# Kernel tuning notes

Measured on AMD Instinct MI355X. Metric: run time of the kernel, lower is better.

Reference implementation:

```python
import jax, jax.numpy as jnp
import numpy as np
from jax import lax

D_MODEL = 768
D_INNER = 1536   # expand * d_model
D_STATE = 16
D_CONV = 4
DT_RANK = 48     # ceil(768/16)
BATCH, SEQLEN = 2, 1024


def silu(x):
    return x * jax.nn.sigmoid(x)


def causal_conv1d(x, w, b):
    # x: (B, L, d)  w: (d, K) depthwise  b: (d,)
    # matches torch Conv1d(groups=d, padding=K-1)[..., :L]
    K = w.shape[1]
    L = x.shape[1]
    xp = jnp.pad(x, ((0, 0), (K - 1, 0), (0, 0)))
    out = b
    for k in range(K):
        out = out + xp[:, k:k + L, :] * w[:, k]
    return out


def mamba_branch(xz, conv_w, conv_b, x_proj_w, dt_proj_w, dt_bias, A_log, D):
    # xz: (B, L, 2*d_inner); faithful to mamba_inner_fn_no_out_proj
    x, z = jnp.split(xz, 2, axis=-1)
    x = silu(causal_conv1d(x, conv_w, conv_b))
    x_dbl = x @ x_proj_w.T                                  # (B,L,dt_rank+2N)
    dt, Bc, Cc = jnp.split(x_dbl, [DT_RANK, DT_RANK + D_STATE], axis=-1)
    delta = jax.nn.softplus(dt @ dt_proj_w.T + dt_bias)     # (B,L,d)
    A = -jnp.exp(A_log)                                     # (d,N)
    dA = jnp.exp(delta[..., None] * A)                      # (B,L,d,N)
    dBx = (delta * x)[..., None] * Bc[:, :, None, :]        # (B,L,d,N)

    def step(h, inp):
        da, dbx = inp
        h = da * h + dbx
        return h, h

    h0 = jnp.zeros((x.shape[0], x.shape[2], D_STATE), x.dtype)
    _, hs = lax.scan(step, h0, (jnp.swapaxes(dA, 0, 1), jnp.swapaxes(dBx, 0, 1)))
    y = jnp.einsum('lbdn,bln->bld', hs, Cc) + x * D         # (B,L,d)
    return y * silu(z)


def setup_inputs() -> dict:
    key = jax.random.key(0)
    ks = jax.random.split(key, 16)
    d, dm, n, r, K = D_INNER, D_MODEL, D_STATE, DT_RANK, D_CONV
    A_log = jnp.log(jnp.broadcast_to(jnp.arange(1, n + 1, dtype=jnp.float32), (d, n)))
    # faithful dt bias init: inverse-softplus of log-uniform dt in [1e-3, 1e-1]
    def dt_bias(k):
        dt = jnp.exp(jax.random.uniform(k, (d,)) * (np.log(0.1) - np.log(0.001)) + np.log(0.001))
        dt = jnp.clip(dt, 1e-4)
        return dt + jnp.log(-jnp.expm1(-dt))
    return {
        'hidden_states': jax.random.normal(ks[0], (BATCH, SEQLEN, dm), jnp.float32),
        'in_proj_w': jax.random.normal(ks[1], (2 * d, dm), jnp.float32) / np.sqrt(dm),
        'conv_w': jax.random.normal(ks[2], (d, K), jnp.float32) / np.sqrt(K),
        'conv_b': jax.random.normal(ks[3], (d,), jnp.float32) * 0.02,
        'x_proj_w': jax.random.normal(ks[4], (r + 2 * n, d), jnp.float32) / np.sqrt(d),
        'dt_proj_w': jax.random.uniform(ks[5], (d, r), jnp.float32, -r ** -0.5, r ** -0.5),
        'dt_proj_b': dt_bias(ks[6]),
        'A_log': A_log,
        'D': jnp.ones((d,), jnp.float32),
        'conv_w_b': jax.random.normal(ks[7], (d, K), jnp.float32) / np.sqrt(K),
        'conv_b_b': jax.random.normal(ks[8], (d,), jnp.float32) * 0.02,
        'x_proj_w_b': jax.random.normal(ks[9], (r + 2 * n, d), jnp.float32) / np.sqrt(d),
        'dt_proj_w_b': jax.random.uniform(ks[10], (d, r), jnp.float32, -r ** -0.5, r ** -0.5),
        'dt_proj_b_b': dt_bias(ks[11]),
        'A_b_log': A_log,
        'D_b': jnp.ones((d,), jnp.float32),
        'out_proj_w': jax.random.normal(ks[12], (dm, d), jnp.float32) / np.sqrt(d),
    }


def reference(hidden_states, in_proj_w, conv_w, conv_b, x_proj_w, dt_proj_w, dt_proj_b,
              A_log, D, conv_w_b, conv_b_b, x_proj_w_b, dt_proj_w_b, dt_proj_b_b,
              A_b_log, D_b, out_proj_w):
    # bimamba v2: forward scan + backward (flipped) scan, summed, then out_proj
    xz = hidden_states @ in_proj_w.T                        # (B,L,2*d_inner)
    out_f = mamba_branch(xz, conv_w, conv_b, x_proj_w, dt_proj_w, dt_proj_b, A_log, D)
    out_r = mamba_branch(xz[:, ::-1, :], conv_w_b, conv_b_b, x_proj_w_b,
                         dt_proj_w_b, dt_proj_b_b, A_b_log, D_b)[:, ::-1, :]
    return (out_f + out_r) @ out_proj_w.T                   # (B,L,d_model)
```

## Files before the change

kernel.cpp:

```cpp
#include <hip/hip_runtime.h>
#include <hip/hip_bf16.h>

#define LL 1024
#define DI 1536
#define N2 3072
#define ML 2048
#define CHUNKS 64
#define CLEN 16

typedef __attribute__((ext_vector_type(8))) short short8;
typedef __attribute__((ext_vector_type(4))) float f4;
typedef __attribute__((ext_vector_type(4))) float f32x4;

__device__ __forceinline__ ushort f2bf(float f) {
  union { float f; unsigned u; } v; v.f = f;
  unsigned u = v.u;
  u += 0x7fffu + ((u >> 16) & 1u);
  return (ushort)(u >> 16);
}
__device__ __forceinline__ float bf2f(ushort u) {
  union { unsigned i; float f; } w; w.i = ((unsigned)u) << 16; return w.f;
}
__device__ __forceinline__ f4 bf2f4(ushort4 u) {
  f4 r; r.x = bf2f(u.x); r.y = bf2f(u.y); r.z = bf2f(u.z); r.w = bf2f(u.w);
  return r;
}

__device__ __forceinline__ void gload16(const ushort* g, ushort* l) {
  __builtin_amdgcn_global_load_lds(
      (const __attribute__((address_space(1))) unsigned int*)g,
      (__attribute__((address_space(3))) unsigned int*)l, 16, 0, 0);
}

struct CvtSeg { const float* s; ushort* d; int n4; };
struct Cvt5 { CvtSeg seg[5]; };

#define CVT_BLOCKS 5232

__global__ void k_cvt(Cvt5 p, int total4,
                      const float* __restrict__ wf, const float* __restrict__ wb,
                      ushort* __restrict__ dtw) {
  int bid = blockIdx.x;
  if (bid < CVT_BLOCKS) {
    int i = bid * 256 + threadIdx.x;
    if (i >= total4) return;
    int off = i, sidx = 0;
    while (sidx < 4 && off >= p.seg[sidx].n4) { off -= p.seg[sidx].n4; ++sidx; }
    f4 v = *(const f4*)(p.seg[sidx].s + (size_t)off * 4);
    ushort4 o;
    o.x = f2bf(v.x); o.y = f2bf(v.y); o.z = f2bf(v.z); o.w = f2bf(v.w);
    *(ushort4*)(p.seg[sidx].d + (size_t)off * 4) = o;
  } else {
    int i = (bid - CVT_BLOCKS) * 256 + threadIdx.x;
    int c = i & 63;
    int rr = i >> 6;
    int dir = rr / 1536;
    int r = rr - dir * 1536;
    const float* w = dir ? wb : wf;
    dtw[i] = (c < 48) ? f2bf(w[r * 48 + c]) : (ushort)0;
  }
}

template<int EPI, bool NGUARD, int KS, bool OBF>
__global__ __launch_bounds__(256)
void k_gemm(const ushort* __restrict__ A, const ushort* __restrict__ Bm,
            void* __restrict__ Cp, int M, int N, int K,
            const float* __restrict__ bias, const float* __restrict__ bias2,
            size_t sA, size_t sB, size_t sC, size_t sKs, int kLen) {
  const int dir = blockIdx.z;
  A += (size_t)dir * sA;
  Bm += (size_t)dir * sB;
  size_t cbase = (size_t)dir * sC;
  const float* bp = (EPI == 1) ? (dir ? bias2 : bias) : nullptr;

  int n0, kOff, kEnd;
  if (KS > 1) {
    int yb_ = blockIdx.y;
    int nt = yb_ / KS, ks = yb_ - nt * KS;
    n0 = nt * 128;
    kOff = ks * kLen;
    kEnd = kOff + kLen;
    cbase += (size_t)ks * sKs;
  } else {
    n0 = blockIdx.y * 128;
    kOff = 0;
    kEnd = K;
  }

  __shared__ ushort As[128 * 32];
  __shared__ ushort Bs[128 * 32];
  const int tid = threadIdx.x;
  const int m0 = blockIdx.x * 128;
  const int wv = tid >> 6;
  const int lane = tid & 63;
  const int wr = (wv >> 1) * 64;
  const int wc = (wv & 1) * 64;
  const int lr = lane & 15;
  const int lk = lane >> 4;
  f32x4 acc[4][4] = {};
  for (int k0 = kOff; k0 < kEnd; k0 += 32) {
    #pragma unroll
    for (int i = 0; i < 2; ++i) {
      int e = (tid + i * 256) * 8;
      int r = e >> 5;
      int c = e & 31;
      gload16(A + (size_t)(m0 + r) * K + k0 + c, &As[(i * 256 + wv * 64) * 8]);
      gload16(Bm + (size_t)(n0 + r) * K + k0 + c, &Bs[(i * 256 + wv * 64) * 8]);
    }
    __syncthreads();
    short8 af[4], bfr[4];
    #pragma unroll
    for (int m = 0; m < 4; ++m) af[m] = *(const short8*)(&As[(wr + m*16 + lr) * 32 + lk*8]);
    #pragma unroll
    for (int n = 0; n < 4; ++n) bfr[n] = *(const short8*)(&Bs[(wc + n*16 + lr) * 32 + lk*8]);
    #pragma unroll
    for (int m = 0; m < 4; ++m)
      #pragma unroll
      for (int n = 0; n < 4; ++n)
        acc[m][n] = __builtin_amdgcn_mfma_f32_16x16x32_bf16(af[m], bfr[n], acc[m][n], 0, 0, 0);
    __syncthreads();
  }
  #pragma unroll
  for (int m = 0; m < 4; ++m) {
    int gr = m0 + wr + m * 16 + lk * 4;
    #pragma unroll
    for (int n = 0; n < 4; ++n) {
      int gc = n0 + wc + n * 16 + lr;
      if (NGUARD && gc >= N) continue;
      #pragma unroll
      for (int r = 0; r < 4; ++r) {
        float v = acc[m][n][r];
        if (EPI == 1) {
          v += bp[gc];
          v = (v > 20.f) ? v : log1pf(__expf(v));
        }
        size_t idx = cbase + (size_t)(gr + r) * N + gc;
        if (OBF) ((ushort*)Cp)[idx] = f2bf(v);
        else     ((float*)Cp)[idx] = v;
      }
    }
  }
}

__global__ void k_xred(const float* __restrict__ partial,
                       float* __restrict__ dtBC, ushort* __restrict__ dtbf) {
  int i = blockIdx.x * 256 + threadIdx.x;
  int dir = i / 40960;
  int rem = i - dir * 40960;
  int row = rem / 20;
  int c4 = rem - row * 20;
  f4 s = {0.f, 0.f, 0.f, 0.f};
  #pragma unroll
  for (int ks = 0; ks < 8; ++ks) {
    f4 v = *(const f4*)(partial + (((size_t)(dir * 8 + ks) * 2048 + row) * 80 + c4 * 4));
    s.x += v.x; s.y += v.y; s.z += v.z; s.w += v.w;
  }
  *(f4*)(dtBC + ((size_t)dir * 163840 + (size_t)row * 80 + c4 * 4)) = s;
  if (c4 < 16) {
    ushort4 u;
    if (c4 < 12) { u.x = f2bf(s.x); u.y = f2bf(s.y); u.z = f2bf(s.z); u.w = f2bf(s.w); }
    else { u.x = 0; u.y = 0; u.z = 0; u.w = 0; }
    *(ushort4*)(dtbf + ((size_t)dir * 131072 + (size_t)row * 64 + c4 * 4)) = u;
  }
}

__global__ void k_ored(const float* __restrict__ part, float* __restrict__ out) {
  int i = blockIdx.x * 256 + threadIdx.x;
  f4 s = {0.f, 0.f, 0.f, 0.f};
  #pragma unroll
  for (int ks = 0; ks < 4; ++ks) {
    f4 v = *(const f4*)(part + (size_t)ks * 1572864 + (size_t)i * 4);
    s.x += v.x; s.y += v.y; s.z += v.z; s.w += v.w;
  }
  *(f4*)(out + (size_t)i * 4) = s;
}

#define CONV_R 8
__global__ __launch_bounds__(192)
void k_conv2(const ushort* __restrict__ xz,
             const float* __restrict__ wf, const float* __restrict__ bf_,
             const float* __restrict__ wb, const float* __restrict__ bb_,
             ushort* __restrict__ xcbf) {
  int d4 = blockIdx.z * 192 + threadIdx.x;
  int b = blockIdx.y;
  int l0 = blockIdx.x * CONV_R;
  int d = d4 * 4;
  f4 w0[4], w1[4];
  #pragma unroll
  for (int c = 0; c < 4; ++c) {
    w0[c] = *(const f4*)(wf + (size_t)d * 4 + c * 4);
    w1[c] = *(const f4*)(wb + (size_t)d * 4 + c * 4);
  }
  f4 bias0 = *(const f4*)(bf_ + d);
  f4 bias1 = *(const f4*)(bb_ + d);
  f4 win[CONV_R + 6];
  #pragma unroll
  for (int j = 0; j < CONV_R + 6; ++j) {
    int t = l0 - 3 + j;
    if (t >= 0 && t < LL) {
      win[j] = bf2f4(*(const ushort4*)(xz + ((size_t)(b * LL + t)) * N2 + d));
    } else {
      f4 z = {0.f, 0.f, 0.f, 0.f};
      win[j] = z;
    }
  }
  #pragma unroll
  for (int i = 0; i < CONV_R; ++i) {
    int l = l0 + i;
    float a0[4], a1[4];
    #pragma unroll
    for (int c = 0; c < 4; ++c) { a0[c] = bias0[c]; a1[c] = bias1[c]; }
    #pragma unroll
    for (int k = 0; k < 4; ++k) {
      f4 xv0 = win[i + k];
      f4 xv1 = win[i + 3 + k];
      #pragma unroll
      for (int c = 0; c < 4; ++c) {
        a0[c] += xv0[c] * w0[c][k];
        a1[c] += xv1[c] * w1[c][3 - k];
      }
    }
    ushort4 o0, o1;
    #pragma unroll
    for (int c = 0; c < 4; ++c) {
      a0[c] = a0[c] / (1.f + __expf(-a0[c]));
      a1[c] = a1[c] / (1.f + __expf(-a1[c]));
    }
    o0.x = f2bf(a0[0]); o0.y = f2bf(a0[1]); o0.z = f2bf(a0[2]); o0.w = f2bf(a0[3]);
    o1.x = f2bf(a1[0]); o1.y = f2bf(a1[1]); o1.z = f2bf(a1[2]); o1.w = f2bf(a1[3]);
    *(ushort4*)(xcbf + ((size_t)(b * LL + l)) * DI + d) = o0;
    *(ushort4*)(xcbf + ((size_t)(ML + b * LL + (LL - 1 - l))) * DI + d) = o1;
  }
}

__global__ __launch_bounds__(256)
void k_scan1(const ushort* __restrict__ delta_all,
             const ushort* __restrict__ xc_all,
             const float* __restrict__ dtBC_all,
             const float* __restrict__ Alog_f, const float* __restrict__ Alog_b,
             float* __restrict__ hL, float* __restrict__ Sv) {
  int dirb = blockIdx.z;
  int dir = dirb >> 1, b = dirb & 1;
  int ch = blockIdx.y;
  int d = blockIdx.x * 256 + threadIdx.x;
  const float* Alog = dir ? Alog_b : Alog_f;
  float Av[16];
  #pragma unroll
  for (int n = 0; n < 16; ++n) Av[n] = -__expf(Alog[d * 16 + n]);
  int l0 = ch * CLEN;
  size_t base = ((size_t)dir * ML + (size_t)b * LL + l0) * DI + d;
  const ushort* dptr = delta_all + base;
  const ushort* xptr = xc_all + base;
  const float* bc = dtBC_all + ((size_t)dir * ML + (size_t)b * LL + l0) * 80 + 48;
  float h[16];
  #pragma unroll
  for (int n = 0; n < 16; ++n) h[n] = 0.f;
  float s = 0.f;
  ushort dln = dptr[0], xvn = xptr[0];
  #pragma unroll 4
  for (int l = 0; l < CLEN; ++l) {
    float dl = bf2f(dln);
    float xv = bf2f(xvn);
    if (l + 1 < CLEN) {
      dln = dptr[(size_t)(l + 1) * DI];
      xvn = xptr[(size_t)(l + 1) * DI];
    }
    float dbx = dl * xv;
    s += dl;
    const float* bp = bc + l * 80;
    #pragma unroll
    for (int q = 0; q < 4; ++q) {
      f4 Bv = *(const f4*)(bp + q * 4);
      #pragma unroll
      for (int j = 0; j < 4; ++j) {
        int n = q * 4 + j;
        h[n] = __expf(dl * Av[n]) * h[n] + dbx * Bv[j];
      }
    }
  }
  size_t si = (((size_t)dirb * CHUNKS + ch) * 1536 + d) * 16;
  #pragma unroll
  for (int q = 0; q < 4; ++q) {
    f4 hv = {h[q*4], h[q*4+1], h[q*4+2], h[q*4+3]};
    *(f4*)(hL + si + q * 4) = hv;
  }
  Sv[((size_t)dirb * CHUNKS + ch) * 1536 + d] = s;
}

__global__ void k_comb(const float* __restrict__ hL, const float* __restrict__ Sv,
                       const float* __restrict__ Alog_f, const float* __restrict__ Alog_b,
                       float* __restrict__ hIn) {
  int tid = blockIdx.x * 256 + threadIdx.x;
  int dirb = tid / 24576;
  int e = tid - dirb * 24576;
  int d = e >> 4;
  const float* Alog = (dirb >> 1) ? Alog_b : Alog_f;
  float Av = -__expf(Alog[e]);
  size_t hbase = (size_t)dirb * CHUNKS * 24576 + e;
  size_t sbase = (size_t)dirb * CHUNKS * 1536 + d;
  float h = 0.f;
  #pragma unroll 8
  for (int ch = 0; ch < CHUNKS; ++ch) {
    hIn[hbase + (size_t)ch * 24576] = h;
    float Pv = __expf(Av * Sv[sbase + (size_t)ch * 1536]);
    h = Pv * h + hL[hbase + (size_t)ch * 24576];
  }
}

__global__ __launch_bounds__(256)
void k_scan2(const ushort* __restrict__ delta_all,
             const ushort* __restrict__ xc_all,
             const float* __restrict__ dtBC_all,
             const float* __restrict__ Alog_f, const float* __restrict__ Df,
             const float* __restrict__ Alog_b, const float* __restrict__ Db,
             const float* __restrict__ hIn,
             ushort* __restrict__ yf, ushort* __restrict__ yb) {
  int dirb = blockIdx.z;
  int dir = dirb >> 1, b = dirb & 1;
  int ch = blockIdx.y;
  int d = blockIdx.x * 256 + threadIdx.x;
  const float* Alog = dir ? Alog_b : Alog_f;
  const float* Dp = dir ? Db : Df;
  float Av[16];
  #pragma unroll
  for (int n = 0; n < 16; ++n) Av[n] = -__expf(Alog[d * 16 + n]);
  float Dvv = Dp[d];
  int l0 = ch * CLEN;
  size_t base = ((size_t)dir * ML + (size_t)b * LL + l0) * DI + d;
  const ushort* dptr = delta_all + base;
  const ushort* xptr = xc_all + base;
  const float* bc = dtBC_all + ((size_t)dir * ML + (size_t)b * LL + l0) * 80 + 48;
  ushort* yo = dir ? yb : yf;
  size_t si = (((size_t)dirb * CHUNKS + ch) * 1536 + d) * 16;
  float h[16];
  #pragma unroll
  for (int q = 0; q < 4; ++q) {
    f4 hv = *(const f4*)(hIn + si + q * 4);
    h[q*4] = hv.x; h[q*4+1] = hv.y; h[q*4+2] = hv.z; h[q*4+3] = hv.w;
  }
  ushort dln = dptr[0], xvn = xptr[0];
  #pragma unroll 4
  for (int l = 0; l < CLEN; ++l) {
    float dl = bf2f(dln);
    float xv = bf2f(xvn);
    if (l + 1 < CLEN) {
      dln = dptr[(size_t)(l + 1) * DI];
      xvn = xptr[(size_t)(l + 1) * DI];
    }
    float dbx = dl * xv;
    const float* bp = bc + l * 80;
    float pr0 = 0.f, pr1 = 0.f, pr2 = 0.f, pr3 = 0.f;
    #pragma unroll
    for (int q = 0; q < 4; ++q) {
      f4 Bv = *(const f4*)(bp + q * 4);
      f4 Cv = *(const f4*)(bp + 16 + q * 4);
      float pq = 0.f;
      #pragma unroll
      for (int j = 0; j < 4; ++j) {
        int n = q * 4 + j;
        h[n] = __expf(dl * Av[n]) * h[n] + dbx * Bv[j];
        pq += h[n] * Cv[j];
      }
      if (q == 0) pr0 = pq; else if (q == 1) pr1 = pq;
      else if (q == 2) pr2 = pq; else pr3 = pq;
    }
    float pr = (pr0 + pr1) + (pr2 + pr3);
    int gl = l0 + l;
    int lo = dir ? (LL - 1 - gl) : gl;
    yo[((size_t)b * LL + lo) * DI + d] = f2bf(pr + xv * Dvv);
  }
}

__global__ void k_gate(const ushort* __restrict__ a, const ushort* __restrict__ b,
                       const ushort* __restrict__ xz, ushort* __restrict__ o) {
  int i = blockIdx.x * 256 + threadIdx.x;
  int row = i / 384;
  int c4 = i - row * 384;
  f4 va = bf2f4(*(const ushort4*)(a + (size_t)i * 4));
  f4 vb = bf2f4(*(const ushort4*)(b + (size_t)i * 4));
  f4 vz = bf2f4(*(const ushort4*)(xz + (size_t)row * N2 + DI + c4 * 4));
  ushort4 u;
  float s0 = vz.x / (1.f + __expf(-vz.x));
  float s1 = vz.y / (1.f + __expf(-vz.y));
  float s2 = vz.z / (1.f + __expf(-vz.z));
  float s3 = vz.w / (1.f + __expf(-vz.w));
  u.x = f2bf((va.x + vb.x) * s0);
  u.y = f2bf((va.y + vb.y) * s1);
  u.z = f2bf((va.z + vb.z) * s2);
  u.w = f2bf((va.w + vb.w) * s3);
  *(ushort4*)(o + (size_t)i * 4) = u;
}

extern "C" void kernel_launch(void* const* d_in, const int* in_sizes, int n_in,
                              void* d_out, int out_size, void* d_ws, size_t ws_size,
                              hipStream_t stream) {
  const float* hidden      = (const float*)d_in[0];
  const float* in_proj_w   = (const float*)d_in[1];
  const float* conv_w      = (const float*)d_in[2];
  const float* conv_b      = (const float*)d_in[3];
  const float* x_proj_w    = (const float*)d_in[4];
  const float* dt_proj_w   = (const float*)d_in[5];
  const float* dt_proj_b   = (const float*)d_in[6];
  const float* A_log       = (const float*)d_in[7];
  const float* Dv          = (const float*)d_in[8];
  const float* conv_w_b    = (const float*)d_in[9];
  const float* conv_b_b    = (const float*)d_in[10];
  const float* x_proj_w_b  = (const float*)d_in[11];
  const float* dt_proj_w_b = (const float*)d_in[12];
  const float* dt_proj_b_b = (const float*)d_in[13];
  const float* A_b_log     = (const float*)d_in[14];
  const float* D_b         = (const float*)d_in[15];
  const float* out_proj_w  = (const float*)d_in[16];
  float* out = (float*)d_out;

  float* wsf   = (float*)d_ws;
  float* dtBC  = wsf;
  float* hL    = wsf + 327680;
  float* Sv    = wsf + 6619136;
  float* hIn   = wsf + 7012352;
  float* xpart = wsf + 327680;
  float* opart = wsf + 327680;
  ushort* wsb      = (ushort*)((char*)d_ws + 53215232);
  ushort* hid_bf   = wsb;
  ushort* win_bf   = wsb + 1572864;
  ushort* xw_bf    = wsb + 3932160;
  ushort* dtw_bf   = wsb + 4177920;
  ushort* wout_bf  = wsb + 4374528;
  ushort* xz_bf    = wsb + 5554176;
  ushort* xc_bf    = wsb + 11845632;
  ushort* dt_bf    = wsb + 18137088;
  ushort* delta_bf = wsb + 18399232;
  ushort* ybf_f    = wsb + 24690688;
  ushort* ybf_b    = wsb + 27836416;
  ushort* y_bf     = wsb + 30982144;
  if (ws_size < 121470976) return;

  Cvt5 c5;
  c5.seg[0] = { hidden,      hid_bf,            1572864 / 4 };
  c5.seg[1] = { in_proj_w,   win_bf,            2359296 / 4 };
  c5.seg[2] = { x_proj_w,    xw_bf,             122880 / 4 };
  c5.seg[3] = { x_proj_w_b,  xw_bf + 122880,    122880 / 4 };
  c5.seg[4] = { out_proj_w,  wout_bf,           1179648 / 4 };
  k_cvt<<<CVT_BLOCKS + 768, 256, 0, stream>>>(c5, 1339392, dt_proj_w, dt_proj_w_b, dtw_bf);

  k_gemm<0, false, 1, true><<<dim3(16, 24), 256, 0, stream>>>(
      hid_bf, win_bf, xz_bf, 2048, 3072, 768, nullptr, nullptr, 0, 0, 0, 0, 0);

  k_conv2<<<dim3(LL / CONV_R, 2, 2), 192, 0, stream>>>(
      xz_bf, conv_w, conv_b, conv_w_b, conv_b_b, xc_bf);

  k_gemm<0, true, 8, false><<<dim3(16, 8, 2), 256, 0, stream>>>(
      xc_bf, xw_bf, xpart, 2048, 80, 1536, nullptr, nullptr,
      3145728, 122880, 1310720, 163840, 192);
  k_xred<<<320, 256, 0, stream>>>(xpart, dtBC, dt_bf);

  k_gemm<1, false, 1, true><<<dim3(16, 12, 2), 256, 0, stream>>>(
      dt_bf, dtw_bf, delta_bf, 2048, 1536, 64, dt_proj_b, dt_proj_b_b,
      131072, 98304, 3145728, 0, 0);

  k_scan1<<<dim3(6, CHUNKS, 4), 256, 0, stream>>>(delta_bf, xc_bf, dtBC,
                                                  A_log, A_b_log, hL, Sv);
  k_comb<<<384, 256, 0, stream>>>(hL, Sv, A_log, A_b_log, hIn);
  k_scan2<<<dim3(6, CHUNKS, 4), 256, 0, stream>>>(delta_bf, xc_bf, dtBC,
                                                  A_log, Dv, A_b_log, D_b, hIn, ybf_f, ybf_b);

  k_gate<<<3072, 256, 0, stream>>>(ybf_f, ybf_b, xz_bf, y_bf);

  k_gemm<0, false, 4, false><<<dim3(16, 24), 256, 0, stream>>>(
      y_bf, wout_bf, opart, 2048, 768, 1536, nullptr, nullptr,
      0, 0, 0, 1572864, 384);
  k_ored<<<1536, 256, 0, stream>>>(opart, out);
}
```

Measured before the change: 262.3 us.

## Fuse gating into out_proj GEMM A-load and store chunk states in bf16

Removes the separate k_gate kernel: the out_proj GEMM now builds its A tile on the fly from y_forward + y_backward times silu(z), writing straight into shared memory instead of using the async global-to-LDS load. Separately, the per-chunk scan states hL and hIn are stored in bf16 instead of fp32, halving that intermediate traffic. The fused load recomputes the sigmoid for every N-tile and K-split block, reading three inputs per element with synchronous loads, which may slow the GEMM main loop. bf16 chunk states also lower the precision of the carried recurrence.

New measurement: 267.9 us. 2.1% more time.

```diff
diff --git a/kernel.cpp b/kernel.cpp
--- a/kernel.cpp
+++ b/kernel.cpp
@@ -61,12 +61,14 @@
   }
 }
 
-template<int EPI, bool NGUARD, int KS, bool OBF>
+template<int EPI, bool NGUARD, int KS, bool OBF, bool AGATE>
 __global__ __launch_bounds__(256)
 void k_gemm(const ushort* __restrict__ A, const ushort* __restrict__ Bm,
             void* __restrict__ Cp, int M, int N, int K,
             const float* __restrict__ bias, const float* __restrict__ bias2,
-            size_t sA, size_t sB, size_t sC, size_t sKs, int kLen) {
+            size_t sA, size_t sB, size_t sC, size_t sKs, int kLen,
+            const ushort* __restrict__ Yf, const ushort* __restrict__ Yb,
+            const ushort* __restrict__ Zz) {
   const int dir = blockIdx.z;
   A += (size_t)dir * sA;
   Bm += (size_t)dir * sB;
@@ -104,7 +106,23 @@
       int e = (tid + i * 256) * 8;
       int r = e >> 5;
       int c = e & 31;
-      gload16(A + (size_t)(m0 + r) * K + k0 + c, &As[(i * 256 + wv * 64) * 8]);
+      if (AGATE) {
+        size_t ro = (size_t)(m0 + r);
+        short8 vf = *(const short8*)(Yf + ro * 1536 + k0 + c);
+        short8 vb = *(const short8*)(Yb + ro * 1536 + k0 + c);
+        short8 vz = *(const short8*)(Zz + ro * 3072 + 1536 + k0 + c);
+        short8 o;
+        #pragma unroll
+        for (int j = 0; j < 8; ++j) {
+          float a = bf2f((ushort)vf[j]) + bf2f((ushort)vb[j]);
+          float zz = bf2f((ushort)vz[j]);
+          float sg = zz / (1.f + __expf(-zz));
+          o[j] = (short)f2bf(a * sg);
+        }
+        *(short8*)(&As[e]) = o;
+      } else {
+        gload16(A + (size_t)(m0 + r) * K + k0 + c, &As[(i * 256 + wv * 64) * 8]);
+      }
       gload16(Bm + (size_t)(n0 + r) * K + k0 + c, &Bs[(i * 256 + wv * 64) * 8]);
     }
     __syncthreads();
@@ -238,7 +256,7 @@
              const ushort* __restrict__ xc_all,
              const float* __restrict__ dtBC_all,
              const float* __restrict__ Alog_f, const float* __restrict__ Alog_b,
-             float* __restrict__ hL, float* __restrict__ Sv) {
+             ushort* __restrict__ hL, float* __restrict__ Sv) {
   int dirb = blockIdx.z;
   int dir = dirb >> 1, b = dirb & 1;
   int ch = blockIdx.y;
@@ -281,15 +299,17 @@
   size_t si = (((size_t)dirb * CHUNKS + ch) * 1536 + d) * 16;
   #pragma unroll
   for (int q = 0; q < 4; ++q) {
-    f4 hv = {h[q*4], h[q*4+1], h[q*4+2], h[q*4+3]};
-    *(f4*)(hL + si + q * 4) = hv;
+    ushort4 hv;
+    hv.x = f2bf(h[q*4]); hv.y = f2bf(h[q*4+1]);
+    hv.z = f2bf(h[q*4+2]); hv.w = f2bf(h[q*4+3]);
+    *(ushort4*)(hL + si + q * 4) = hv;
   }
   Sv[((size_t)dirb * CHUNKS + ch) * 1536 + d] = s;
 }
 
-__global__ void k_comb(const float* __restrict__ hL, const float* __restrict__ Sv,
+__global__ void k_comb(const ushort* __restrict__ hL, const float* __restrict__ Sv,
                        const float* __restrict__ Alog_f, const float* __restrict__ Alog_b,
-                       float* __restrict__ hIn) {
+                       ushort* __restrict__ hIn) {
   int tid = blockIdx.x * 256 + threadIdx.x;
   int dirb = tid / 24576;
   int e = tid - dirb * 24576;
@@ -301,9 +321,9 @@
   float h = 0.f;
   #pragma unroll 8
   for (int ch = 0; ch < CHUNKS; ++ch) {
-    hIn[hbase + (size_t)ch * 24576] = h;
+    hIn[hbase + (size_t)ch * 24576] = f2bf(h);
     float Pv = __expf(Av * Sv[sbase + (size_t)ch * 1536]);
-    h = Pv * h + hL[hbase + (size_t)ch * 24576];
+    h = Pv * h + bf2f(hL[hbase + (size_t)ch * 24576]);
   }
 }
 
@@ -313,7 +333,7 @@
              const float* __restrict__ dtBC_all,
              const float* __restrict__ Alog_f, const float* __restrict__ Df,
              const float* __restrict__ Alog_b, const float* __restrict__ Db,
-             const float* __restrict__ hIn,
+             const ushort* __restrict__ hIn,
              ushort* __restrict__ yf, ushort* __restrict__ yb) {
   int dirb = blockIdx.z;
   int dir = dirb >> 1, b = dirb & 1;
@@ -335,8 +355,9 @@
   float h[16];
   #pragma unroll
   for (int q = 0; q < 4; ++q) {
-    f4 hv = *(const f4*)(hIn + si + q * 4);
-    h[q*4] = hv.x; h[q*4+1] = hv.y; h[q*4+2] = hv.z; h[q*4+3] = hv.w;
+    ushort4 hv = *(const ushort4*)(hIn + si + q * 4);
+    h[q*4] = bf2f(hv.x); h[q*4+1] = bf2f(hv.y);
+    h[q*4+2] = bf2f(hv.z); h[q*4+3] = bf2f(hv.w);
   }
   ushort dln = dptr[0], xvn = xptr[0];
   #pragma unroll 4
@@ -369,26 +390,6 @@
     int lo = dir ? (LL - 1 - gl) : gl;
     yo[((size_t)b * LL + lo) * DI + d] = f2bf(pr + xv * Dvv);
   }
-}
-
-__global__ void k_gate(const ushort* __restrict__ a, const ushort* __restrict__ b,
-                       const ushort* __restrict__ xz, ushort* __restrict__ o) {
-  int i = blockIdx.x * 256 + threadIdx.x;
-  int row = i / 384;
-  int c4 = i - row * 384;
-  f4 va = bf2f4(*(const ushort4*)(a + (size_t)i * 4));
-  f4 vb = bf2f4(*(const ushort4*)(b + (size_t)i * 4));
-  f4 vz = bf2f4(*(const ushort4*)(xz + (size_t)row * N2 + DI + c4 * 4));
-  ushort4 u;
-  float s0 = vz.x / (1.f + __expf(-vz.x));
-  float s1 = vz.y / (1.f + __expf(-vz.y));
-  float s2 = vz.z / (1.f + __expf(-vz.z));
-  float s3 = vz.w / (1.f + __expf(-vz.w));
-  u.x = f2bf((va.x + vb.x) * s0);
-  u.y = f2bf((va.y + vb.y) * s1);
-  u.z = f2bf((va.z + vb.z) * s2);
-  u.w = f2bf((va.w + vb.w) * s3);
-  *(ushort4*)(o + (size_t)i * 4) = u;
 }
 
 extern "C" void kernel_launch(void* const* d_in, const int* in_sizes, int n_in,
@@ -415,12 +416,10 @@
 
   float* wsf   = (float*)d_ws;
   float* dtBC  = wsf;
-  float* hL    = wsf + 327680;
-  float* Sv    = wsf + 6619136;
-  float* hIn   = wsf + 7012352;
-  float* xpart = wsf + 327680;
-  float* opart = wsf + 327680;
-  ushort* wsb      = (ushort*)((char*)d_ws + 53215232);
+  float* Sv    = wsf + 327680;
+  float* xpart = wsf + 720896;
+  float* opart = wsf + 720896;
+  ushort* wsb      = (ushort*)((char*)d_ws + 28049408);
   ushort* hid_bf   = wsb;
   ushort* win_bf   = wsb + 1572864;
   ushort* xw_bf    = wsb + 3932160;
@@ -432,8 +431,9 @@
   ushort* delta_bf = wsb + 18399232;
   ushort* ybf_f    = wsb + 24690688;
   ushort* ybf_b    = wsb + 27836416;
-  ushort* y_bf     = wsb + 30982144;
-  if (ws_size < 121470976) return;
+  ushort* hL_bf    = wsb + 30982144;
+  ushort* hIn_bf   = wsb + 37273600;
+  if (ws_size < 115179520) return;
 
   Cvt5 c5;
   c5.seg[0] = { hidden,      hid_bf,            1572864 / 4 };
@@ -443,31 +443,31 @@
   c5.seg[4] = { out_proj_w,  wout_bf,           1179648 / 4 };
   k_cvt<<<CVT_BLOCKS + 768, 256, 0, stream>>>(c5, 1339392, dt_proj_w, dt_proj_w_b, dtw_bf);
 
-  k_gemm<0, false, 1, true><<<dim3(16, 24), 256, 0, stream>>>(
-      hid_bf, win_bf, xz_bf, 2048, 3072, 768, nullptr, nullptr, 0, 0, 0, 0, 0);
+  k_gemm<0, false, 1, true, false><<<dim3(16, 24), 256, 0, stream>>>(
+      hid_bf, win_bf, xz_bf, 2048, 3072, 768, nullptr, nullptr,
+      0, 0, 0, 0, 0, nullptr, nullptr, nullptr);
 
   k_conv2<<<dim3(LL / CONV_R, 2, 2), 192, 0, stream>>>(
       xz_bf, conv_w, conv_b, conv_w_b, conv_b_b, xc_bf);
 
-  k_gemm<0, true, 8, false><<<dim3(16, 8, 2), 256, 0, stream>>>(
+  k_gemm<0, true, 8, false, false><<<dim3(16, 8, 2), 256, 0, stream>>>(
       xc_bf, xw_bf, xpart, 2048, 80, 1536, nullptr, nullptr,
-      3145728, 122880, 1310720, 163840, 192);
+      3145728, 122880, 1310720, 163840, 192, nullptr, nullptr, nullptr);
   k_xred<<<320, 256, 0, stream>>>(xpart, dtBC, dt_bf);
 
-  k_gemm<1, false, 1, true><<<dim3(16, 12, 2), 256, 0, stream>>>(
+  k_gemm<1, false, 1, true, false><<<dim3(16, 12, 2), 256, 0, stream>>>(
       dt_bf, dtw_bf, delta_bf, 2048, 1536, 64, dt_proj_b, dt_proj_b_b,
-      131072, 98304, 3145728, 0, 0);
+      131072, 98304, 3145728, 0, 0, nullptr, nullptr, nullptr);
 
   k_scan1<<<dim3(6, CHUNKS, 4), 256, 0, stream>>>(delta_bf, xc_bf, dtBC,
-                                                  A_log, A_b_log, hL, Sv);
-  k_comb<<<384, 256, 0, stream>>>(hL, Sv, A_log, A_b_log, hIn);
+                                                  A_log, A_b_log, hL_bf, Sv);
+  k_comb<<<384, 256, 0, stream>>>(hL_bf, Sv, A_log, A_b_log, hIn_bf);
   k_scan2<<<dim3(6, CHUNKS, 4), 256, 0, stream>>>(delta_bf, xc_bf, dtBC,
-                                                  A_log, Dv, A_b_log, D_b, hIn, ybf_f, ybf_b);
-
-  k_gate<<<3072, 256, 0, stream>>>(ybf_f, ybf_b, xz_bf, y_bf);
-
-  k_gemm<0, false, 4, false><<<dim3(16, 24), 256, 0, stream>>>(
-      y_bf, wout_bf, opart, 2048, 768, 1536, nullptr, nullptr,
-      0, 0, 0, 1572864, 384);
+                                                  A_log, Dv, A_b_log, D_b,
+                                                  hIn_bf, ybf_f, ybf_b);
+
+  k_gemm<0, false, 4, false, true><<<dim3(16, 24), 256, 0, stream>>>(
+      nullptr, wout_bf, opart, 2048, 768, 1536, nullptr, nullptr,
+      0, 0, 0, 1572864, 384, ybf_f, ybf_b, xz_bf);
   k_ored<<<1536, 256, 0, stream>>>(opart, out);
 }
```
